# Performance work log

Measured on AMD Instinct MI355X. Metric: run time of the kernel, lower is better.

## Reference

```python
import jax, jax.numpy as jnp
import numpy as np

CONF_THRES = 0.25   # NMS.conf
IOU_THRES = 0.45    # NMS.iou
MAX_NMS = 1024      # fixed candidate count so greedy NMS is jit-compatible
IMG = 640.0


def setup_inputs() -> dict:
    key = jax.random.key(0)
    k0, k1, k2, k3, k4 = jax.random.split(key, 5)
    B, N = 32, 25200
    cxcy = jax.random.uniform(k0, (B, N, 2), dtype=jnp.float32) * IMG
    wh = jax.random.uniform(k1, (B, N, 2), dtype=jnp.float32) * 80.0 + 2.0
    obj = jax.random.uniform(k2, (B, N, 1), dtype=jnp.float32)
    lmk = jax.random.uniform(k3, (B, N, 10), dtype=jnp.float32) * IMG
    cls = jax.random.uniform(k4, (B, N, 1), dtype=jnp.float32)
    # layout: [cx, cy, w, h, obj, 10 landmark coords, 1 class score]
    prediction = jnp.concatenate([cxcy, wh, obj, lmk, cls], axis=2)
    return {"prediction": prediction}


def xywh2xyxy(x):
    cx, cy, w, h = x[:, 0], x[:, 1], x[:, 2], x[:, 3]
    return jnp.stack([cx - w / 2, cy - h / 2, cx + w / 2, cy + h / 2], axis=1)


def pairwise_iou(b):  # b: [K,4] xyxy -> [K,K]
    area = (b[:, 2] - b[:, 0]) * (b[:, 3] - b[:, 1])
    lt = jnp.maximum(b[:, None, :2], b[None, :, :2])
    rb = jnp.minimum(b[:, None, 2:], b[None, :, 2:])
    wh = jnp.clip(rb - lt, 0.0)
    inter = wh[..., 0] * wh[..., 1]
    return inter / (area[:, None] + area[None, :] - inter + 1e-7)


def _nms_image(pred):  # pred: [N,16]
    obj = pred[:, 4]
    score = pred[:, 15] * obj  # x[:,15:] *= x[:,4:5]; nc==1 -> single class, j==0
    valid = (obj > CONF_THRES) & (score > CONF_THRES)  # xc filter + conf filter
    s = jnp.where(valid, score, -1.0)
    top_s, idx = jax.lax.top_k(s, MAX_NMS)  # score-sorted candidates (greedy NMS order)
    x = pred[idx]  # [K,16]
    box = xywh2xyxy(x[:, :4])
    vmask = top_s > 0.0  # valid candidates (invalid slots carry score -1)
    # class offset c = j*4096 is identically 0 since nc==1 -> skip
    iou = pairwise_iou(box)  # [K,K]
    rng = jnp.arange(MAX_NMS)

    def step(keep, i):
        sup = keep[i] & (iou[i] > IOU_THRES) & (rng > i)
        return keep & ~sup, None

    keep, _ = jax.lax.scan(step, vmask, rng)
    det = jnp.concatenate(
        [box, top_s[:, None], x[:, 5:15], jnp.zeros((MAX_NMS, 1), pred.dtype)], axis=1
    )  # [K,16] = box(4) | conf(1) | landmarks(10) | class(1)=0
    return det * keep[:, None].astype(det.dtype), keep


def reference(prediction):
    # Fixed-shape analogue of the per-image ragged output: detections padded to
    # MAX_NMS rows per image (zeroed where suppressed) plus a keep mask.
    det, keep = jax.vmap(_nms_image)(prediction)
    return det, keep
```

## Files before the change

### kernel.cpp

```cpp
#include <hip/hip_runtime.h>
#include <stdint.h>

#define NB 32
#define NN 25200
#define NN4 6300
#define TOPK 1024
#define NF 16
#define CONF 0.25f
#define IOU_T 0.45f
#define NBIN 4096
#define CAP 2048
#define KEY_BASE 0xBE800001u
#define PITCH 257
#define CSTRIDE 32

__device__ __forceinline__ uint32_t score_key(float obj, float cls) {
  float score = __fmul_rn(cls, obj);
  bool valid = (obj > CONF) && (score > CONF);
  float s = valid ? score : -1.0f;
  uint32_t u = __float_as_uint(s);
  return (u & 0x80000000u) ? ~u : (u | 0x80000000u);
}

__device__ __forceinline__ uint64_t shfl_xor_u64(uint64_t v, int m) {
  uint32_t lo = __shfl_xor((uint32_t)v, m, 64);
  uint32_t hi = __shfl_xor((uint32_t)(v >> 32), m, 64);
  return ((uint64_t)hi << 32) | lo;
}

__global__ void k_keys(const float* __restrict__ pred, uint32_t* __restrict__ keys,
                       uint32_t* __restrict__ cnt) {
  if (blockIdx.x == 0) {
    #pragma unroll
    for (int q = 0; q < 4; ++q) cnt[threadIdx.x + q * 256] = 0u;
  }
  int g = blockIdx.x * blockDim.x + threadIdx.x;
  if (g >= NB * NN) return;
  const float* row = pred + (size_t)g * NF;
  keys[g] = score_key(row[4], row[15]);
}

__global__ __launch_bounds__(1024) void k_select(const float* __restrict__ pred,
                                                 const uint32_t* __restrict__ keys,
                                                 int* __restrict__ sel,
                                                 float4* __restrict__ boxv,
                                                 float* __restrict__ arv,
                                                 uint32_t* __restrict__ vb) {
  int b = blockIdx.x;
  int tid = threadIdx.x;
  int lane = tid & 63, wid = tid >> 6;
  const uint4* kb4 = (const uint4*)(keys + (size_t)b * NN);
  __shared__ uint32_t hist[NBIN];
  __shared__ uint64_t ent[CAP];
  __shared__ uint32_t wsum[16];
  __shared__ uint32_t sh_bin;
  __shared__ uint32_t sh_cnt;
  #pragma unroll
  for (int k = 0; k < 4; ++k) hist[tid + 1024 * k] = 0;
  ent[tid] = 0; ent[tid + 1024] = 0;
  if (tid == 0) { sh_cnt = 0; sh_bin = 0; }
  __syncthreads();

  uint4 kreg[7];
  #pragma unroll
  for (int k = 0; k < 7; ++k) {
    int i = tid + k * 1024;
    if (i < NN4) {
      kreg[k] = kb4[i];
      uint32_t kv[4] = {kreg[k].x, kreg[k].y, kreg[k].z, kreg[k].w};
      #pragma unroll
      for (int c = 0; c < 4; ++c) {
        uint32_t key = kv[c];
        if (key >= KEY_BASE) {
          uint32_t bin = (key - KEY_BASE) >> 12;
          if (bin > NBIN - 1) bin = NBIN - 1;
          atomicAdd(&hist[bin], 1u);
        }
      }
    }
  }
  __syncthreads();

  uint32_t h[4]; uint32_t s = 0;
  #pragma unroll
  for (int k = 0; k < 4; ++k) { h[k] = hist[NBIN - 1 - (4 * tid + k)]; s += h[k]; }
  uint32_t my = s;
  #pragma unroll
  for (int d = 1; d < 64; d <<= 1) {
    uint32_t v = __shfl_up(s, d, 64);
    if (lane >= d) s += v;
  }
  if (lane == 63) wsum[wid] = s;
  __syncthreads();
  uint32_t base = 0;
  for (int w = 0; w < wid; ++w) base += wsum[w];
  uint32_t cum = base + s - my;
  #pragma unroll
  for (int k = 0; k < 4; ++k) {
    if (cum < TOPK && cum + h[k] >= TOPK) sh_bin = (uint32_t)(NBIN - 1 - (4 * tid + k));
    cum += h[k];
  }
  __syncthreads();
  uint32_t thr = KEY_BASE + (sh_bin << 12);

  #pragma unroll
  for (int k = 0; k < 7; ++k) {
    int i = tid + k * 1024;
    if (i < NN4) {
      uint32_t kv[4] = {kreg[k].x, kreg[k].y, kreg[k].z, kreg[k].w};
      #pragma unroll
      for (int c = 0; c < 4; ++c) {
        uint32_t key = kv[c];
        if (key >= thr) {
          uint32_t p = atomicAdd(&sh_cnt, 1u);
          if (p < CAP) ent[p] = ((uint64_t)key << 32) | (uint32_t)(~(uint32_t)(4 * i + c));
        }
      }
    }
  }
  __syncthreads();

  uint64_t v0 = ent[tid], v1 = ent[tid + 1024];
  for (unsigned kk = 2; kk <= CAP; kk <<= 1) {
    for (unsigned j = kk >> 1; j > 0; j >>= 1) {
      if (j == 1024) {
        uint64_t mx = v0 > v1 ? v0 : v1;
        uint64_t mn = v0 > v1 ? v1 : v0;
        v0 = mx; v1 = mn;
      } else if (j >= 64) {
        __syncthreads();
        ent[tid] = v0; ent[tid + 1024] = v1;
        __syncthreads();
        uint64_t p0 = ent[tid ^ j], p1 = ent[(tid ^ j) + 1024];
        bool low = ((tid & j) == 0);
        bool d0 = ((tid & kk) == 0);
        bool d1 = (((tid + 1024) & kk) == 0);
        v0 = (low != d0) ? (v0 < p0 ? v0 : p0) : (v0 > p0 ? v0 : p0);
        v1 = (low != d1) ? (v1 < p1 ? v1 : p1) : (v1 > p1 ? v1 : p1);
      } else {
        uint64_t p0 = shfl_xor_u64(v0, (int)j);
        uint64_t p1 = shfl_xor_u64(v1, (int)j);
        bool low = ((tid & j) == 0);
        bool d0 = ((tid & kk) == 0);
        bool d1 = (((tid + 1024) & kk) == 0);
        v0 = (low != d0) ? (v0 < p0 ? v0 : p0) : (v0 > p0 ? v0 : p0);
        v1 = (low != d1) ? (v1 < p1 ? v1 : p1) : (v1 > p1 ? v1 : p1);
      }
    }
  }
  uint32_t key = (uint32_t)(v0 >> 32);
  uint32_t n = ~(uint32_t)(v0 & 0xFFFFFFFFu);
  if (n >= NN) n = 0;
  sel[(size_t)b * TOPK + tid] = (int)n;

  bool valid = key >= KEY_BASE;
  uint64_t bal = __ballot(valid);
  if (lane == 0) {
    vb[(size_t)b * 32 + 2 * wid] = (uint32_t)bal;
    vb[(size_t)b * 32 + 2 * wid + 1] = (uint32_t)(bal >> 32);
  }

  {
    const float4* row = (const float4*)(pred + ((size_t)b * NN + n) * NF);
    float4 r0 = row[0];
    float hw = __fmul_rn(r0.z, 0.5f), hh = __fmul_rn(r0.w, 0.5f);
    float x1 = __fsub_rn(r0.x, hw), y1 = __fsub_rn(r0.y, hh);
    float x2 = __fadd_rn(r0.x, hw), y2 = __fadd_rn(r0.y, hh);
    boxv[(size_t)b * TOPK + tid] = make_float4(x1, y1, x2, y2);
    arv[(size_t)b * TOPK + tid] = __fmul_rn(__fsub_rn(x2, x1), __fsub_rn(y2, y1));
  }
}

__global__ __launch_bounds__(1024, 4) void k_maskscan(const float* __restrict__ pred,
                                                      const int* __restrict__ sel,
                                                      const float4* __restrict__ boxv,
                                                      const float* __restrict__ arv,
                                                      const uint32_t* __restrict__ vb,
                                                      uint32_t* __restrict__ mask,
                                                      uint32_t* __restrict__ cnt,
                                                      float* __restrict__ det,
                                                      float* __restrict__ keep_out) {
  int b = blockIdx.x;
  int sblk = blockIdx.y;
  int tid = threadIdx.x;
  int rg = tid & 31;
  int cc = tid >> 5;
  __shared__ uint4 sm4[32 * PITCH];
  __shared__ uint32_t part[1024];
  __shared__ uint32_t Kvec[32];
  __shared__ uint32_t vbs[32];
  __shared__ uint32_t sflag;
  float* bx1 = (float*)sm4;
  float* by1 = bx1 + TOPK;
  float* bx2 = by1 + TOPK;
  float* by2 = bx2 + TOPK;
  float* bar = by2 + TOPK;

  uint32_t* cntm = cnt + (size_t)b * CSTRIDE;

  {
    float4 bb = boxv[(size_t)b * TOPK + tid];
    bx1[tid] = bb.x; by1[tid] = bb.y; bx2[tid] = bb.z; by2[tid] = bb.w;
    bar[tid] = arv[(size_t)b * TOPK + tid];
  }
  __syncthreads();
  int q = (rg < 16) ? (32 * sblk + rg) : (32 * (7 - sblk) + rg);
  int i0 = 4 * q;
  int iw = q >> 3;
  uint32_t wreg[4] = {0u, 0u, 0u, 0u};
  if (cc >= iw) {
    float rx1[4], ry1[4], rx2[4], ry2[4], rar[4];
    #pragma unroll
    for (int k = 0; k < 4; ++k) {
      rx1[k] = bx1[i0 + k]; ry1[k] = by1[i0 + k];
      rx2[k] = bx2[i0 + k]; ry2[k] = by2[i0 + k]; rar[k] = bar[i0 + k];
    }
    for (int jj = 0; jj < 32; ++jj) {
      int j = cc * 32 + jj;
      float cx1 = bx1[j], cy1 = by1[j], cx2 = bx2[j], cy2 = by2[j], car = bar[j];
      #pragma unroll
      for (int k = 0; k < 4; ++k) {
        float lx = fmaxf(rx1[k], cx1);
        float ly = fmaxf(ry1[k], cy1);
        float rx = fminf(rx2[k], cx2);
        float ry = fminf(ry2[k], cy2);
        float wd = fmaxf(__fsub_rn(rx, lx), 0.0f);
        float ht = fmaxf(__fsub_rn(ry, ly), 0.0f);
        float inter = __fmul_rn(wd, ht);
        float den = __fadd_rn(__fsub_rn(__fadd_rn(rar[k], car), inter), 1e-7f);
        float iou = __fdiv_rn(inter, den);
        wreg[k] |= (iou > IOU_T ? 1u : 0u) << jj;
      }
    }
    if (cc == iw) {
      #pragma unroll
      for (int k = 0; k < 4; ++k)
        wreg[k] &= ~((2u << ((i0 + k) & 31)) - 1u);
    }
  }
  {
    uint4 out = make_uint4(wreg[0], wreg[1], wreg[2], wreg[3]);
    *(uint4*)&mask[((size_t)b * 32 + cc) * TOPK + i0] = out;
  }

  __syncthreads();
  if (tid == 0)
    __hip_atomic_fetch_add(cntm, 1u, __ATOMIC_RELEASE, __HIP_MEMORY_SCOPE_AGENT);
  if (sblk != 0) return;

  uint32_t kw0 = 0;
  if (tid < 32) kw0 = vb[(size_t)b * 32 + tid];
  int n = sel[(size_t)b * TOPK + tid];
  const float4* rowv = (const float4*)(pred + ((size_t)b * NN + n) * NF);
  float4 r0 = rowv[0], r1 = rowv[1], r2 = rowv[2], r3 = rowv[3];

  if (tid == 0) {
    while (__hip_atomic_load(cntm, __ATOMIC_RELAXED, __HIP_MEMORY_SCOPE_AGENT) < 8u)
      __builtin_amdgcn_s_sleep(16);
    (void)__hip_atomic_load(cntm, __ATOMIC_ACQUIRE, __HIP_MEMORY_SCOPE_AGENT);
  }
  __syncthreads();

  const uint4* gm4 = (const uint4*)(mask + (size_t)b * (32 * TOPK));
  #pragma unroll
  for (int qq = 0; qq < 8; ++qq) {
    int idx4 = tid + qq * 1024;
    int row = idx4 >> 8;
    int col4 = idx4 & 255;
    sm4[row * PITCH + col4] = gm4[idx4];
  }
  if (tid < 32) { vbs[tid] = kw0; Kvec[tid] = kw0; }
  __syncthreads();

  {
    int l = tid & 31;
    int chunk = tid >> 5;
    const int rbase = l * PITCH + chunk * 8;
    uint32_t go = 1u;
    for (int sweep = 0; sweep < 1030 && go; ++sweep) {
      uint32_t kc = Kvec[chunk];
      uint32_t acc = 0;
      #pragma unroll
      for (int qq = 0; qq < 8; ++qq) {
        uint4 v = sm4[rbase + qq];
        acc |= (0u - ((kc >> (qq * 4 + 0)) & 1u)) & v.x;
        acc |= (0u - ((kc >> (qq * 4 + 1)) & 1u)) & v.y;
        acc |= (0u - ((kc >> (qq * 4 + 2)) & 1u)) & v.z;
        acc |= (0u - ((kc >> (qq * 4 + 3)) & 1u)) & v.w;
      }
      part[tid] = acc;
      __syncthreads();
      if (tid < 32) {
        uint32_t red = 0;
        #pragma unroll
        for (int c = 0; c < 32; ++c) red |= part[c * 32 + tid];
        uint32_t nk = vbs[tid] & ~red;
        uint64_t chg = __ballot(nk != Kvec[tid]);
        Kvec[tid] = nk;
        if (tid == 0) sflag = (chg != 0ull) ? 1u : 0u;
      }
      __syncthreads();
      go = sflag;
    }
  }

  bool kept = (Kvec[tid >> 5] >> (tid & 31)) & 1u;
  float m = kept ? 1.0f : 0.0f;
  float score = __fmul_rn(r3.w, r1.x);
  float hw = __fmul_rn(r0.z, 0.5f), hh = __fmul_rn(r0.w, 0.5f);
  float4 o0 = make_float4(__fsub_rn(r0.x, hw) * m, __fsub_rn(r0.y, hh) * m,
                          __fadd_rn(r0.x, hw) * m, __fadd_rn(r0.y, hh) * m);
  float4 o1 = make_float4(score * m, r1.y * m, r1.z * m, r1.w * m);
  float4 o2 = make_float4(r2.x * m, r2.y * m, r2.z * m, r2.w * m);
  float4 o3 = make_float4(r3.x * m, r3.y * m, r3.z * m, 0.0f);
  float4* dst = (float4*)(det + ((size_t)b * TOPK + tid) * NF);
  dst[0] = o0; dst[1] = o1; dst[2] = o2; dst[3] = o3;
  keep_out[(size_t)b * TOPK + tid] = m;
}

extern "C" void kernel_launch(void* const* d_in, const int* in_sizes, int n_in,
                              void* d_out, int out_size, void* d_ws, size_t ws_size,
                              hipStream_t stream) {
  const float* pred = (const float*)d_in[0];
  float* det = (float*)d_out;
  float* keep = det + (size_t)NB * TOPK * NF;

  uint8_t* ws = (uint8_t*)d_ws;
  size_t off = 0;
  uint32_t* keys = (uint32_t*)(ws + off); off += (size_t)NB * NN * 4;
  int* sel = (int*)(ws + off);            off += (size_t)NB * TOPK * 4;
  uint32_t* mask = (uint32_t*)(ws + off); off += (size_t)NB * 32 * TOPK * 4;
  float4* boxv = (float4*)(ws + off);     off += (size_t)NB * TOPK * 16;
  float* arv = (float*)(ws + off);        off += (size_t)NB * TOPK * 4;
  uint32_t* vb = (uint32_t*)(ws + off);   off += (size_t)NB * 32 * 4;
  uint32_t* cnt = (uint32_t*)(ws + off);  off += (size_t)NB * CSTRIDE * 4;

  k_keys<<<(NB * NN + 255) / 256, 256, 0, stream>>>(pred, keys, cnt);
  k_select<<<NB, 1024, 0, stream>>>(pred, keys, sel, boxv, arv, vb);
  dim3 gm(NB, 8);
  k_maskscan<<<gm, 1024, 0, stream>>>(pred, sel, boxv, arv, vb, mask, cnt, det, keep);
}
```

Before: 146.5 us.

## Fuse top-k selection into the mask/scan kernel, recomputing selection per block

Merges the per-image selection kernel (histogram threshold plus bitonic sort) into the IoU-mask/greedy-scan kernel. Each of the 8 blocks per image now redoes the top-k selection in its own LDS, aliased onto the mask buffer, and builds the box arrays directly in shared memory. This removes one kernel launch and the global round trip for selected indices, boxes, areas and valid bits. In exchange the selection work and the key reads run eight times per image instead of once.

```diff
diff --git a/kernel.cpp b/kernel.cpp
--- a/kernel.cpp
+++ b/kernel.cpp
@@ -40,21 +40,39 @@
   keys[g] = score_key(row[4], row[15]);
 }
 
-__global__ __launch_bounds__(1024) void k_select(const float* __restrict__ pred,
+__global__ __launch_bounds__(1024, 4) void k_nms(const float* __restrict__ pred,
                                                  const uint32_t* __restrict__ keys,
-                                                 int* __restrict__ sel,
-                                                 float4* __restrict__ boxv,
-                                                 float* __restrict__ arv,
-                                                 uint32_t* __restrict__ vb) {
+                                                 uint32_t* __restrict__ mask,
+                                                 uint32_t* __restrict__ cnt,
+                                                 float* __restrict__ det,
+                                                 float* __restrict__ keep_out) {
   int b = blockIdx.x;
+  int sblk = blockIdx.y;
   int tid = threadIdx.x;
   int lane = tid & 63, wid = tid >> 6;
-  const uint4* kb4 = (const uint4*)(keys + (size_t)b * NN);
-  __shared__ uint32_t hist[NBIN];
-  __shared__ uint64_t ent[CAP];
+  int rg = tid & 31;
+  int cc = tid >> 5;
+
+  __shared__ uint4 sm4[32 * PITCH];
+  __shared__ uint32_t part[1024];
+  __shared__ uint32_t Kvec[32];
+  __shared__ uint32_t vbs[32];
+  __shared__ uint32_t sflag;
   __shared__ uint32_t wsum[16];
   __shared__ uint32_t sh_bin;
   __shared__ uint32_t sh_cnt;
+
+  float* bx1 = (float*)sm4;
+  float* by1 = bx1 + TOPK;
+  float* bx2 = by1 + TOPK;
+  float* by2 = bx2 + TOPK;
+  float* bar = by2 + TOPK;
+  uint32_t* hist = (uint32_t*)(bar + TOPK);
+  uint64_t* ent = (uint64_t*)(hist + NBIN);
+
+  uint32_t* cntm = cnt + (size_t)b * CSTRIDE;
+
+  const uint4* kb4 = (const uint4*)(keys + (size_t)b * NN);
   #pragma unroll
   for (int k = 0; k < 4; ++k) hist[tid + 1024 * k] = 0;
   ent[tid] = 0; ent[tid + 1024] = 0;
@@ -149,15 +167,17 @@
     }
   }
   uint32_t key = (uint32_t)(v0 >> 32);
-  uint32_t n = ~(uint32_t)(v0 & 0xFFFFFFFFu);
-  if (n >= NN) n = 0;
-  sel[(size_t)b * TOPK + tid] = (int)n;
-
-  bool valid = key >= KEY_BASE;
-  uint64_t bal = __ballot(valid);
-  if (lane == 0) {
-    vb[(size_t)b * 32 + 2 * wid] = (uint32_t)bal;
-    vb[(size_t)b * 32 + 2 * wid + 1] = (uint32_t)(bal >> 32);
+  uint32_t nn = ~(uint32_t)(v0 & 0xFFFFFFFFu);
+  if (nn >= NN) nn = 0;
+  int n = (int)nn;
+
+  {
+    bool valid = key >= KEY_BASE;
+    uint64_t bal = __ballot(valid);
+    if (lane == 0) {
+      vbs[2 * wid] = (uint32_t)bal;  vbs[2 * wid + 1] = (uint32_t)(bal >> 32);
+      Kvec[2 * wid] = (uint32_t)bal; Kvec[2 * wid + 1] = (uint32_t)(bal >> 32);
+    }
   }
 
   {
@@ -166,44 +186,11 @@
     float hw = __fmul_rn(r0.z, 0.5f), hh = __fmul_rn(r0.w, 0.5f);
     float x1 = __fsub_rn(r0.x, hw), y1 = __fsub_rn(r0.y, hh);
     float x2 = __fadd_rn(r0.x, hw), y2 = __fadd_rn(r0.y, hh);
-    boxv[(size_t)b * TOPK + tid] = make_float4(x1, y1, x2, y2);
-    arv[(size_t)b * TOPK + tid] = __fmul_rn(__fsub_rn(x2, x1), __fsub_rn(y2, y1));
-  }
-}
-
-__global__ __launch_bounds__(1024, 4) void k_maskscan(const float* __restrict__ pred,
-                                                      const int* __restrict__ sel,
-                                                      const float4* __restrict__ boxv,
-                                                      const float* __restrict__ arv,
-                                                      const uint32_t* __restrict__ vb,
-                                                      uint32_t* __restrict__ mask,
-                                                      uint32_t* __restrict__ cnt,
-                                                      float* __restrict__ det,
-                                                      float* __restrict__ keep_out) {
-  int b = blockIdx.x;
-  int sblk = blockIdx.y;
-  int tid = threadIdx.x;
-  int rg = tid & 31;
-  int cc = tid >> 5;
-  __shared__ uint4 sm4[32 * PITCH];
-  __shared__ uint32_t part[1024];
-  __shared__ uint32_t Kvec[32];
-  __shared__ uint32_t vbs[32];
-  __shared__ uint32_t sflag;
-  float* bx1 = (float*)sm4;
-  float* by1 = bx1 + TOPK;
-  float* bx2 = by1 + TOPK;
-  float* by2 = bx2 + TOPK;
-  float* bar = by2 + TOPK;
-
-  uint32_t* cntm = cnt + (size_t)b * CSTRIDE;
-
-  {
-    float4 bb = boxv[(size_t)b * TOPK + tid];
-    bx1[tid] = bb.x; by1[tid] = bb.y; bx2[tid] = bb.z; by2[tid] = bb.w;
-    bar[tid] = arv[(size_t)b * TOPK + tid];
-  }
-  __syncthreads();
+    bx1[tid] = x1; by1[tid] = y1; bx2[tid] = x2; by2[tid] = y2;
+    bar[tid] = __fmul_rn(__fsub_rn(x2, x1), __fsub_rn(y2, y1));
+  }
+  __syncthreads();
+
   int q = (rg < 16) ? (32 * sblk + rg) : (32 * (7 - sblk) + rg);
   int i0 = 4 * q;
   int iw = q >> 3;
@@ -242,15 +229,11 @@
     uint4 out = make_uint4(wreg[0], wreg[1], wreg[2], wreg[3]);
     *(uint4*)&mask[((size_t)b * 32 + cc) * TOPK + i0] = out;
   }
-
   __syncthreads();
   if (tid == 0)
     __hip_atomic_fetch_add(cntm, 1u, __ATOMIC_RELEASE, __HIP_MEMORY_SCOPE_AGENT);
   if (sblk != 0) return;
 
-  uint32_t kw0 = 0;
-  if (tid < 32) kw0 = vb[(size_t)b * 32 + tid];
-  int n = sel[(size_t)b * TOPK + tid];
   const float4* rowv = (const float4*)(pred + ((size_t)b * NN + n) * NF);
   float4 r0 = rowv[0], r1 = rowv[1], r2 = rowv[2], r3 = rowv[3];
 
@@ -269,7 +252,6 @@
     int col4 = idx4 & 255;
     sm4[row * PITCH + col4] = gm4[idx4];
   }
-  if (tid < 32) { vbs[tid] = kw0; Kvec[tid] = kw0; }
   __syncthreads();
 
   {
@@ -328,15 +310,10 @@
   uint8_t* ws = (uint8_t*)d_ws;
   size_t off = 0;
   uint32_t* keys = (uint32_t*)(ws + off); off += (size_t)NB * NN * 4;
-  int* sel = (int*)(ws + off);            off += (size_t)NB * TOPK * 4;
   uint32_t* mask = (uint32_t*)(ws + off); off += (size_t)NB * 32 * TOPK * 4;
-  float4* boxv = (float4*)(ws + off);     off += (size_t)NB * TOPK * 16;
-  float* arv = (float*)(ws + off);        off += (size_t)NB * TOPK * 4;
-  uint32_t* vb = (uint32_t*)(ws + off);   off += (size_t)NB * 32 * 4;
   uint32_t* cnt = (uint32_t*)(ws + off);  off += (size_t)NB * CSTRIDE * 4;
 
   k_keys<<<(NB * NN + 255) / 256, 256, 0, stream>>>(pred, keys, cnt);
-  k_select<<<NB, 1024, 0, stream>>>(pred, keys, sel, boxv, arv, vb);
-  dim3 gm(NB, 8);
-  k_maskscan<<<gm, 1024, 0, stream>>>(pred, sel, boxv, arv, vb, mask, cnt, det, keep);
-}
+  dim3 g(NB, 8);
+  k_nms<<<g, 1024, 0, stream>>>(pred, keys, mask, cnt, det, keep);
+}
```

New measurement: 142.9 us. 2.5% less time.
